# Performance work log

Measured on AMD Instinct MI355X. Metric: run time of the kernel, lower is better.

The kernel has to match this reference:

```python
import jax, jax.numpy as jnp
import numpy as np

B, N, D, K = 4, 8192, 128, 32
LN_EPS = 1e-5


def setup_inputs() -> dict:
    key = jax.random.key(0)
    k1, k2, k3, k4 = jax.random.split(key, 4)
    x = jax.random.normal(k1, (B, N, D), dtype=jnp.float32)
    adj = jax.random.randint(k2, (B, N, K), 0, N, dtype=jnp.int64)
    W = jax.random.normal(k3, (2 * D, D), dtype=jnp.float32) * (1.0 / np.sqrt(2 * D))
    b = jnp.zeros((D,), dtype=jnp.float32)
    gamma = jnp.ones((D,), dtype=jnp.float32)
    beta = jnp.zeros((D,), dtype=jnp.float32)
    return {"x": x, "adj": adj, "W": W, "b": b, "gamma": gamma, "beta": beta}


def reference(x, adj, W, b, gamma, beta):
    # Gather neighbor features: neigh[b,n,k,:] = x[b, adj[b,n,k], :]
    # (avoids the original's (B,N,N,D) blowup; direct index gather)
    neigh = jnp.take_along_axis(x[:, None, :, :], adj[..., None], axis=2)  # (B,N,K,D)
    neigh_mean = neigh.mean(axis=2)  # (B,N,D)
    h = jnp.concatenate([x, neigh_mean], axis=-1)  # (B,N,2D)
    h = jnp.einsum('bnf,fd->bnd', h, W) + b
    h = jax.nn.gelu(h, approximate=False)
    # dropout is identity in eval mode
    y = h + x
    mu = y.mean(axis=-1, keepdims=True)
    var = y.var(axis=-1, keepdims=True)
    return (y - mu) * jax.lax.rsqrt(var + LN_EPS) * gamma + beta
```

## Files before the change

### kernel.cpp

```cpp
#include <hip/hip_runtime.h>

#define B_ 4
#define N_ 8192
#define D_ 128
#define K_ 32

typedef short short8 __attribute__((ext_vector_type(8)));
typedef float f32x4 __attribute__((ext_vector_type(4)));

__device__ __forceinline__ unsigned short f2bf(float f) {
  unsigned int u = __float_as_uint(f);
  u += 0x7FFFu + ((u >> 16) & 1u);
  return (unsigned short)(u >> 16);
}
__device__ __forceinline__ float bf2f(unsigned short h) {
  return __uint_as_float(((unsigned int)h) << 16);
}

__global__ __launch_bounds__(512) void gemm_kernel(
    const float* __restrict__ x, const float* __restrict__ W,
    float* __restrict__ p1, unsigned short* __restrict__ p2h) {
  __shared__ __align__(16) unsigned char in_tile[32 * 256];

  const int t = threadIdx.x, wave = t >> 6, lane = t & 63;
  const int l15 = lane & 15, kg = lane >> 4;
  const long row0 = (long)blockIdx.x * 32;

  #pragma unroll
  for (int i = 0; i < 2; ++i) {
    int idx = t + i * 512;
    int row = idx >> 5, cs = idx & 31;
    float4 v = *reinterpret_cast<const float4*>(x + (row0 + row) * D_ + cs * 4);
    ushort4 o;
    o.x = f2bf(v.x); o.y = f2bf(v.y); o.z = f2bf(v.z); o.w = f2bf(v.w);
    *reinterpret_cast<ushort4*>(
        in_tile + ((row * 256 + cs * 8) ^ ((row & 7) << 4))) = o;
  }

  const int halfw = wave & 3, is_v = wave >> 2;
  const float* Wb = W + (is_v ? D_ * D_ : 0);
  short8 bw[2][4];
  #pragma unroll
  for (int tt = 0; tt < 2; ++tt)
    #pragma unroll
    for (int ks = 0; ks < 4; ++ks)
      #pragma unroll
      for (int j = 0; j < 8; ++j)
        bw[tt][ks][j] = (short)f2bf(
            Wb[(ks * 32 + kg * 8 + j) * D_ + halfw * 32 + tt * 16 + l15]);
  __syncthreads();

  f32x4 acc[2][2];
  #pragma unroll
  for (int r = 0; r < 2; ++r)
    #pragma unroll
    for (int tt = 0; tt < 2; ++tt)
      acc[r][tt] = (f32x4){0.f, 0.f, 0.f, 0.f};

  #pragma unroll
  for (int ks = 0; ks < 4; ++ks) {
    #pragma unroll
    for (int r = 0; r < 2; ++r) {
      int row = r * 16 + l15;
      short8 af = *reinterpret_cast<const short8*>(
          in_tile + ((row * 256 + ks * 64 + kg * 16) ^ ((row & 7) << 4)));
      acc[r][0] = __builtin_amdgcn_mfma_f32_16x16x32_bf16(af, bw[0][ks], acc[r][0], 0, 0, 0);
      acc[r][1] = __builtin_amdgcn_mfma_f32_16x16x32_bf16(af, bw[1][ks], acc[r][1], 0, 0, 0);
    }
  }

  #pragma unroll
  for (int r = 0; r < 2; ++r)
    #pragma unroll
    for (int tt = 0; tt < 2; ++tt)
      #pragma unroll
      for (int i = 0; i < 4; ++i) {
        int row = r * 16 + kg * 4 + i;
        int col = halfw * 32 + tt * 16 + l15;
        float val = acc[r][tt][i];
        if (!is_v) p1[(row0 + row) * D_ + col] = val;
        else       p2h[(row0 + row) * D_ + col] = f2bf(val);
      }
}

__global__ __launch_bounds__(256) void gather_kernel(
    const int* __restrict__ adj, const float* __restrict__ p1,
    const unsigned short* __restrict__ p2h, const float* __restrict__ x,
    const float* __restrict__ bias, const float* __restrict__ gamma,
    const float* __restrict__ beta, float* __restrict__ out) {
  const int t = threadIdx.x;
  const int wave = t >> 6, lane = t & 63;
  const int vblk = ((blockIdx.x & 7) << 8) + (blockIdx.x >> 3);
  const int node_base = vblk * 16 + wave * 4;
  const int b = node_base >> 13;
  const unsigned int* vb =
      (const unsigned int*)p2h + (size_t)b * (N_ * (D_ / 2));
  const int c0 = lane * 2;
  const float2 bi = *reinterpret_cast<const float2*>(bias + c0);
  const float2 ga = *reinterpret_cast<const float2*>(gamma + c0);
  const float2 be = *reinterpret_cast<const float2*>(beta + c0);
  const int nbu = __builtin_amdgcn_readfirstlane(node_base);

  #pragma unroll
  for (int j = 0; j < 4; ++j) {
    const int gn = nbu + j;
    const int* ap = adj + (size_t)gn * K_;
    float a0 = 0.f, a1 = 0.f;
    #pragma unroll
    for (int k = 0; k < K_; ++k) {
      unsigned int v = vb[(size_t)ap[k] * (D_ / 2) + lane];
      a0 += __uint_as_float(v << 16);
      a1 += __uint_as_float(v & 0xFFFF0000u);
    }
    const float2 u  = *reinterpret_cast<const float2*>(p1 + (size_t)gn * D_ + c0);
    const float2 xv = *reinterpret_cast<const float2*>(x  + (size_t)gn * D_ + c0);
    float h0 = u.x + a0 * 0.03125f + bi.x;
    float h1 = u.y + a1 * 0.03125f + bi.y;
    h0 = 0.5f * h0 * (1.f + erff(h0 * 0.70710678118f));
    h1 = 0.5f * h1 * (1.f + erff(h1 * 0.70710678118f));
    const float y0 = h0 + xv.x, y1 = h1 + xv.y;
    float s = y0 + y1, sq = y0 * y0 + y1 * y1;
    #pragma unroll
    for (int off = 1; off < 64; off <<= 1) {
      s  += __shfl_xor(s, off, 64);
      sq += __shfl_xor(sq, off, 64);
    }
    const float mu   = s * (1.f / 128.f);
    const float rstd = rsqrtf(sq * (1.f / 128.f) - mu * mu + 1e-5f);
    float2 o;
    o.x = (y0 - mu) * rstd * ga.x + be.x;
    o.y = (y1 - mu) * rstd * ga.y + be.y;
    *reinterpret_cast<float2*>(out + (size_t)gn * D_ + c0) = o;
  }
}

__global__ __launch_bounds__(512) void fused_f32_kernel(
    const float* __restrict__ x, const int* __restrict__ adj,
    const float* __restrict__ W, const float* __restrict__ bias,
    const float* __restrict__ gamma, const float* __restrict__ beta,
    float* __restrict__ out) {
  __shared__ __align__(16) unsigned char smem[40960];
  unsigned char* in_tile = smem;
  int* adj_lds = (int*)(smem + 32768);
  float* y = (float*)smem;
  const int t = threadIdx.x, wave = t >> 6, lane = t & 63;
  const int l15 = lane & 15, kg = lane >> 4;
  const int vid = (blockIdx.x & 7) * 64 + (blockIdx.x >> 3);
  const int bidx = vid >> 7;
  const long row0 = (long)bidx * N_ + (vid & 127) * 64;
  #pragma unroll
  for (int i = 0; i < 4; ++i)
    adj_lds[t + i * 512] = adj[row0 * K_ + t + i * 512];
  #pragma unroll
  for (int i = 0; i < 4; ++i) {
    int idx = t + i * 512;
    int row = idx >> 5, cp = (idx & 31) * 4;
    float4 v = *reinterpret_cast<const float4*>(x + (row0 + row) * D_ + cp);
    ushort4 o;
    o.x = f2bf(v.x); o.y = f2bf(v.y); o.z = f2bf(v.z); o.w = f2bf(v.w);
    *reinterpret_cast<ushort4*>(in_tile + row * 512 + ((2 * cp) ^ ((row & 7) << 4))) = o;
  }
  __syncthreads();
  {
    const int g = t & 31, rb = t >> 5, c0 = g * 4;
    #pragma unroll
    for (int batch = 0; batch < 4; ++batch) {
      int row = rb + batch * 16;
      const int* ap = adj_lds + row * K_;
      float a0 = 0, a1 = 0, a2 = 0, a3 = 0;
      for (int k = 0; k < K_; ++k) {
        float4 v = *reinterpret_cast<const float4*>(x + ((long)bidx * N_ + ap[k]) * D_ + c0);
        a0 += v.x; a1 += v.y; a2 += v.z; a3 += v.w;
      }
      ushort4 m;
      m.x = f2bf(a0 * 0.03125f); m.y = f2bf(a1 * 0.03125f);
      m.z = f2bf(a2 * 0.03125f); m.w = f2bf(a3 * 0.03125f);
      *reinterpret_cast<ushort4*>(in_tile + row * 512 +
                                  ((2 * (D_ + c0)) ^ ((row & 7) << 4))) = m;
    }
  }
  __syncthreads();
  const int dl = (wave << 4) + l15;
  f32x4 acc[4];
  #pragma unroll
  for (int r = 0; r < 4; ++r) acc[r] = (f32x4){0.f, 0.f, 0.f, 0.f};
  #pragma unroll
  for (int ks = 0; ks < 8; ++ks) {
    short8 bwk;
    #pragma unroll
    for (int j = 0; j < 8; ++j)
      bwk[j] = (short)f2bf(W[(ks * 32 + kg * 8 + j) * D_ + dl]);
    #pragma unroll
    for (int r = 0; r < 4; ++r) {
      int row = r * 16 + l15;
      short8 af = *reinterpret_cast<const short8*>(
          in_tile + row * 512 + ((2 * (ks * 32 + kg * 8)) ^ ((row & 7) << 4)));
      acc[r] = __builtin_amdgcn_mfma_f32_16x16x32_bf16(af, bwk, acc[r], 0, 0, 0);
    }
  }
  __syncthreads();
  const float bv = bias[dl];
  #pragma unroll
  for (int r = 0; r < 4; ++r)
    #pragma unroll
    for (int i = 0; i < 4; ++i) {
      int row = r * 16 + kg * 4 + i;
      float h = acc[r][i] + bv;
      float ge = 0.5f * h * (1.f + erff(h * 0.70710678118f));
      y[row * 132 + dl] = ge + x[(row0 + row) * D_ + dl];
    }
  __syncthreads();
  {
    const int row = t >> 3, l8 = t & 7;
    const float* yr = y + row * 132 + l8 * 16;
    float4 v[4];
    float s = 0.f, sq = 0.f;
    #pragma unroll
    for (int i = 0; i < 4; ++i) {
      v[i] = *reinterpret_cast<const float4*>(yr + i * 4);
      s += v[i].x + v[i].y + v[i].z + v[i].w;
      sq += v[i].x * v[i].x + v[i].y * v[i].y + v[i].z * v[i].z + v[i].w * v[i].w;
    }
    #pragma unroll
    for (int off = 1; off < 8; off <<= 1) {
      s += __shfl_xor(s, off, 64);
      sq += __shfl_xor(sq, off, 64);
    }
    const float mu = s * (1.f / 128.f);
    const float rstd = rsqrtf(sq * (1.f / 128.f) - mu * mu + 1e-5f);
    float* orow = out + (row0 + row) * D_ + l8 * 16;
    #pragma unroll
    for (int i = 0; i < 4; ++i) {
      float4 g = *reinterpret_cast<const float4*>(gamma + l8 * 16 + i * 4);
      float4 bb = *reinterpret_cast<const float4*>(beta + l8 * 16 + i * 4);
      float4 o;
      o.x = (v[i].x - mu) * rstd * g.x + bb.x;
      o.y = (v[i].y - mu) * rstd * g.y + bb.y;
      o.z = (v[i].z - mu) * rstd * g.z + bb.z;
      o.w = (v[i].w - mu) * rstd * g.w + bb.w;
      *reinterpret_cast<float4*>(orow + i * 4) = o;
    }
  }
}

extern "C" void kernel_launch(void* const* d_in, const int* in_sizes, int n_in,
                              void* d_out, int out_size, void* d_ws, size_t ws_size,
                              hipStream_t stream) {
  const float* x     = (const float*)d_in[0];
  const int*   adj   = (const int*)d_in[1];
  const float* W     = (const float*)d_in[2];
  const float* bias  = (const float*)d_in[3];
  const float* gamma = (const float*)d_in[4];
  const float* beta  = (const float*)d_in[5];
  float* out = (float*)d_out;

  const size_t p1_bytes = (size_t)B_ * N_ * D_ * 4;
  const size_t p2_bytes = (size_t)B_ * N_ * D_ * 2;

  if (ws_size >= p1_bytes + p2_bytes) {
    float* p1 = (float*)d_ws;
    unsigned short* p2h = (unsigned short*)((char*)d_ws + p1_bytes);
    gemm_kernel<<<dim3((B_ * N_) / 32), dim3(512), 0, stream>>>(x, W, p1, p2h);
    gather_kernel<<<dim3(2048), dim3(256), 0, stream>>>(
        adj, p1, p2h, x, bias, gamma, beta, out);
  } else {
    fused_f32_kernel<<<dim3((B_ * N_) / 64), dim3(512), 0, stream>>>(
        x, adj, W, bias, gamma, beta, out);
  }
}
```

Before: 110.3 us.

## Pre-convert W to transposed bf16, double GEMM row tile, interleave bf16 projections

Adds a small kernel that converts W to bf16 once per call in transposed layout, so each GEMM wave loads its B fragments as contiguous 16-byte vectors instead of 32 strided scalar loads with per-element conversion. The GEMM tile grows from 32 to 64 rows per block, spreading the weight-fragment load over more MFMA work. Both projections are now stored as bf16 in one interleaved 256-wide buffer, which cuts the self-projection write and read traffic in half but lowers the precision of that term. The cost is an extra kernel launch and a gather stride that doubles to 512 bytes per row.

```diff
diff --git a/kernel.cpp b/kernel.cpp
--- a/kernel.cpp
+++ b/kernel.cpp
@@ -17,17 +17,25 @@
   return __uint_as_float(((unsigned int)h) << 16);
 }
 
+__global__ __launch_bounds__(256) void cvt_w_kernel(const float* __restrict__ W,
+                                                    unsigned short* __restrict__ Wt) {
+  int e = blockIdx.x * 256 + threadIdx.x;
+  int d = e & 127, fglob = e >> 7;
+  int is_v = fglob >> 7, floc = fglob & 127;
+  Wt[(is_v * 128 + d) * 128 + floc] = f2bf(W[e]);
+}
+
 __global__ __launch_bounds__(512) void gemm_kernel(
-    const float* __restrict__ x, const float* __restrict__ W,
-    float* __restrict__ p1, unsigned short* __restrict__ p2h) {
-  __shared__ __align__(16) unsigned char in_tile[32 * 256];
+    const float* __restrict__ x, const unsigned short* __restrict__ Wt,
+    unsigned short* __restrict__ P) {
+  __shared__ __align__(16) unsigned char in_tile[64 * 256];
 
   const int t = threadIdx.x, wave = t >> 6, lane = t & 63;
   const int l15 = lane & 15, kg = lane >> 4;
-  const long row0 = (long)blockIdx.x * 32;
-
-  #pragma unroll
-  for (int i = 0; i < 2; ++i) {
+  const long row0 = (long)blockIdx.x * 64;
+
+  #pragma unroll
+  for (int i = 0; i < 4; ++i) {
     int idx = t + i * 512;
     int row = idx >> 5, cs = idx & 31;
     float4 v = *reinterpret_cast<const float4*>(x + (row0 + row) * D_ + cs * 4);
@@ -38,21 +46,20 @@
   }
 
   const int halfw = wave & 3, is_v = wave >> 2;
-  const float* Wb = W + (is_v ? D_ * D_ : 0);
   short8 bw[2][4];
   #pragma unroll
-  for (int tt = 0; tt < 2; ++tt)
+  for (int tt = 0; tt < 2; ++tt) {
+    const int col = is_v * 128 + halfw * 32 + tt * 16 + l15;
     #pragma unroll
     for (int ks = 0; ks < 4; ++ks)
-      #pragma unroll
-      for (int j = 0; j < 8; ++j)
-        bw[tt][ks][j] = (short)f2bf(
-            Wb[(ks * 32 + kg * 8 + j) * D_ + halfw * 32 + tt * 16 + l15]);
-  __syncthreads();
-
-  f32x4 acc[2][2];
-  #pragma unroll
-  for (int r = 0; r < 2; ++r)
+      bw[tt][ks] = *reinterpret_cast<const short8*>(
+          Wt + col * 128 + ks * 32 + kg * 8);
+  }
+  __syncthreads();
+
+  f32x4 acc[4][2];
+  #pragma unroll
+  for (int r = 0; r < 4; ++r)
     #pragma unroll
     for (int tt = 0; tt < 2; ++tt)
       acc[r][tt] = (f32x4){0.f, 0.f, 0.f, 0.f};
@@ -60,7 +67,7 @@
   #pragma unroll
   for (int ks = 0; ks < 4; ++ks) {
     #pragma unroll
-    for (int r = 0; r < 2; ++r) {
+    for (int r = 0; r < 4; ++r) {
       int row = r * 16 + l15;
       short8 af = *reinterpret_cast<const short8*>(
           in_tile + ((row * 256 + ks * 64 + kg * 16) ^ ((row & 7) << 4)));
@@ -70,31 +77,30 @@
   }
 
   #pragma unroll
-  for (int r = 0; r < 2; ++r)
-    #pragma unroll
-    for (int tt = 0; tt < 2; ++tt)
+  for (int r = 0; r < 4; ++r)
+    #pragma unroll
+    for (int tt = 0; tt < 2; ++tt) {
+      const int col = is_v * 128 + halfw * 32 + tt * 16 + l15;
       #pragma unroll
       for (int i = 0; i < 4; ++i) {
         int row = r * 16 + kg * 4 + i;
-        int col = halfw * 32 + tt * 16 + l15;
-        float val = acc[r][tt][i];
-        if (!is_v) p1[(row0 + row) * D_ + col] = val;
-        else       p2h[(row0 + row) * D_ + col] = f2bf(val);
+        P[(row0 + row) * 256 + col] = f2bf(acc[r][tt][i]);
       }
+    }
 }
 
 __global__ __launch_bounds__(256) void gather_kernel(
-    const int* __restrict__ adj, const float* __restrict__ p1,
-    const unsigned short* __restrict__ p2h, const float* __restrict__ x,
-    const float* __restrict__ bias, const float* __restrict__ gamma,
-    const float* __restrict__ beta, float* __restrict__ out) {
+    const int* __restrict__ adj, const unsigned short* __restrict__ P,
+    const float* __restrict__ x, const float* __restrict__ bias,
+    const float* __restrict__ gamma, const float* __restrict__ beta,
+    float* __restrict__ out) {
   const int t = threadIdx.x;
   const int wave = t >> 6, lane = t & 63;
   const int vblk = ((blockIdx.x & 7) << 8) + (blockIdx.x >> 3);
   const int node_base = vblk * 16 + wave * 4;
   const int b = node_base >> 13;
-  const unsigned int* vb =
-      (const unsigned int*)p2h + (size_t)b * (N_ * (D_ / 2));
+  const unsigned int* pd = (const unsigned int*)P;
+  const unsigned int* vbase = pd + ((size_t)b << 13) * 128 + 64 + lane;
   const int c0 = lane * 2;
   const float2 bi = *reinterpret_cast<const float2*>(bias + c0);
   const float2 ga = *reinterpret_cast<const float2*>(gamma + c0);
@@ -108,14 +114,14 @@
     float a0 = 0.f, a1 = 0.f;
     #pragma unroll
     for (int k = 0; k < K_; ++k) {
-      unsigned int v = vb[(size_t)ap[k] * (D_ / 2) + lane];
+      unsigned int v = vbase[(size_t)ap[k] * 128];
       a0 += __uint_as_float(v << 16);
       a1 += __uint_as_float(v & 0xFFFF0000u);
     }
-    const float2 u  = *reinterpret_cast<const float2*>(p1 + (size_t)gn * D_ + c0);
-    const float2 xv = *reinterpret_cast<const float2*>(x  + (size_t)gn * D_ + c0);
-    float h0 = u.x + a0 * 0.03125f + bi.x;
-    float h1 = u.y + a1 * 0.03125f + bi.y;
+    const unsigned int ud = pd[(size_t)gn * 128 + lane];
+    const float2 xv = *reinterpret_cast<const float2*>(x + (size_t)gn * D_ + c0);
+    float h0 = __uint_as_float(ud << 16)        + a0 * 0.03125f + bi.x;
+    float h1 = __uint_as_float(ud & 0xFFFF0000u) + a1 * 0.03125f + bi.y;
     h0 = 0.5f * h0 * (1.f + erff(h0 * 0.70710678118f));
     h1 = 0.5f * h1 * (1.f + erff(h1 * 0.70710678118f));
     const float y0 = h0 + xv.x, y1 = h1 + xv.y;
@@ -254,15 +260,16 @@
   const float* beta  = (const float*)d_in[5];
   float* out = (float*)d_out;
 
-  const size_t p1_bytes = (size_t)B_ * N_ * D_ * 4;
-  const size_t p2_bytes = (size_t)B_ * N_ * D_ * 2;
-
-  if (ws_size >= p1_bytes + p2_bytes) {
-    float* p1 = (float*)d_ws;
-    unsigned short* p2h = (unsigned short*)((char*)d_ws + p1_bytes);
-    gemm_kernel<<<dim3((B_ * N_) / 32), dim3(512), 0, stream>>>(x, W, p1, p2h);
+  const size_t p_bytes  = (size_t)B_ * N_ * 256 * 2;
+  const size_t wt_bytes = (size_t)256 * 128 * 2;
+
+  if (ws_size >= p_bytes + wt_bytes) {
+    unsigned short* P  = (unsigned short*)d_ws;
+    unsigned short* Wt = (unsigned short*)((char*)d_ws + p_bytes);
+    cvt_w_kernel<<<dim3(128), dim3(256), 0, stream>>>(W, Wt);
+    gemm_kernel<<<dim3((B_ * N_) / 64), dim3(512), 0, stream>>>(x, Wt, P);
     gather_kernel<<<dim3(2048), dim3(256), 0, stream>>>(
-        adj, p1, p2h, x, bias, gamma, beta, out);
+        adj, P, x, bias, gamma, beta, out);
   } else {
     fused_f32_kernel<<<dim3((B_ * N_) / 64), dim3(512), 0, stream>>>(
         x, adj, W, bias, gamma, beta, out);
```

After: 108.4 us. No clear change (-1.7%).
